# Performance work log

Measured on AMD Instinct MI355X. Metric: run time of the kernel, lower is better.

## Reference

```python
import jax, jax.numpy as jnp
import numpy as np


def setup_inputs() -> dict:
    key = jax.random.key(0)
    ks = jax.random.split(key, 9)
    B = 1024
    s = 0.05
    return {
        "x": jax.random.normal(ks[0], (B, 1024), dtype=jnp.float32),
        "u1": jax.random.normal(ks[1], (8, 8, 16), dtype=jnp.float32) * s,
        "u2": jax.random.normal(ks[2], (8, 8, 16), dtype=jnp.float32) * s,
        "u3": jax.random.normal(ks[3], (16, 16, 16), dtype=jnp.float32) * s,
        "b2": jax.random.normal(ks[4], (16, 16, 16), dtype=jnp.float32) * s,
        "b1_core": jax.random.normal(ks[5], (16, 16), dtype=jnp.float32) * s,
        "bias1": jax.random.normal(ks[6], (8, 8, 16), dtype=jnp.float32) * s,
        "fc2_w": jax.random.normal(ks[7], (10, 1024), dtype=jnp.float32) * s,
        "fc2_b": jax.random.normal(ks[8], (10,), dtype=jnp.float32) * s,
    }


def reference(x, u1, u2, u3, b2, b1_core, bias1, fc2_w, fc2_b):
    batch = x.shape[0]
    t = x.reshape(batch, 8, 8, 16)                       # z a b c
    t = jnp.einsum('zabc,ade->zbcde', t, u1)             # (z,8,16,8,16)
    t = jnp.einsum('zabcd,def->zabcef', t, b2)           # (z,8,16,8,16,16)
    t = jnp.einsum('zabcde,afd->zbcef', t, u2)           # (z,16,8,16,8)
    t = jnp.einsum('zabcd,ce->zabde', t, b1_core)        # (z,16,8,8,16)
    t = jnp.einsum('zabcd,aed->zbce', t, u3)             # (z,8,8,16)
    t = t + bias1
    h = jax.nn.relu(t.reshape(batch, 1024))
    return h @ fc2_w.T + fc2_b
```

## Files before the change

kernel.cpp:

```cpp
#include <hip/hip_runtime.h>


using s16x8 = __attribute__((ext_vector_type(8))) short;
using f32x4 = __attribute__((ext_vector_type(4))) float;

__device__ inline short f2bf(float f) {
    unsigned u = __builtin_bit_cast(unsigned, f);
    u += 0x7fffu + ((u >> 16) & 1u);
    return (short)(u >> 16);
}

__global__ __launch_bounds__(256) void k_build_w(
    const float* __restrict__ u1, const float* __restrict__ u2,
    const float* __restrict__ u3, const float* __restrict__ b2,
    const float* __restrict__ b1c, const float* __restrict__ fc2b,
    short* __restrict__ Wb, float* __restrict__ out) {
    const int blk = blockIdx.x;
    const int tid = threadIdx.x;
    if (blk >= 256) {
        int idx = (blk - 256) * 256 + tid;
        out[idx] = fc2b[idx % 10];
        return;
    }
    __shared__ float b1s[256];
    __shared__ float C2f[4096];
    __shared__ float T1s[256];
    __shared__ float T2s[1024];
    const int ad = blk >> 2, quarter = blk & 3;
    b1s[tid] = b1c[tid];
    __syncthreads();
    for (int j = 0; j < 16; ++j) {
        int idx = tid + 256 * j;
        int e = idx >> 8, p = (idx >> 4) & 15, s = idx & 15;
        float acc = 0.f;
#pragma unroll
        for (int q = 0; q < 16; ++q)
            acc += b2[e * 256 + p * 16 + q] * b1s[q * 16 + s];
        C2f[idx] = acc;
    }
    __syncthreads();
    {
        float acc = 0.f;
#pragma unroll
        for (int e = 0; e < 16; ++e)
            acc += u1[ad * 16 + e] * C2f[e * 256 + tid];
        T1s[tid] = acc;
    }
    __syncthreads();
    for (int j = 0; j < 4; ++j) {
        int idx = tid + 256 * j;
        int s = idx & 15, r = (idx >> 4) & 7, b = idx >> 7;
        float acc = 0.f;
#pragma unroll
        for (int p = 0; p < 16; ++p)
            acc += T1s[p * 16 + s] * u2[(b * 8 + r) * 16 + p];
        T2s[idx] = acc;
    }
    __syncthreads();
    const int a = ad >> 3, d = ad & 7;
    const int rt = quarter * 32 + (tid >> 3);
    const int r = rt >> 4, t = rt & 15;
    const int b = tid & 7;
    const float* t2p = &T2s[(b * 8 + r) * 16];
    short* wrow = &Wb[(d * 128 + rt) * 1024 + a * 128 + b * 16];
    s16x8 v0, v1;
#pragma unroll
    for (int c = 0; c < 16; ++c) {
        const float* u3p = &u3[c * 256 + t * 16];
        float acc = 0.f;
#pragma unroll
        for (int s = 0; s < 16; ++s) acc += t2p[s] * u3p[s];
        short bf = f2bf(acc);
        if (c < 8) v0[c] = bf; else v1[c - 8] = bf;
    }
    *(s16x8*)(wrow) = v0;
    *(s16x8*)(wrow + 8) = v1;
}

#define LDK 136

__global__ __launch_bounds__(256) void k_gemm(
    const float* __restrict__ X, const short* __restrict__ Wb,
    const float* __restrict__ bias, const float* __restrict__ W2,
    float* __restrict__ out) {
    __shared__ short As[64][LDK];
    __shared__ short Bs[64][LDK];
    __shared__ float W2s[10][64];
    const int tid = threadIdx.x;
    const int lane = tid & 63;
    const int w = tid >> 6, wr = w >> 1, wc = w & 1;
    const int z0 = blockIdx.y * 64, o0 = blockIdx.x * 64;
    const int srow = tid >> 2;
    const int sc = (tid & 3) * 16;

    if (tid < 160) {
        int jj = (tid * 4) >> 6, c = (tid * 4) & 63;
        *(float4*)&W2s[jj][c] = *(const float4*)&W2[jj * 1024 + o0 + c];
    }

    const float* xp = &X[(z0 + srow) * 1024 + sc];
    const short* wp = &Wb[(o0 + srow) * 1024 + sc];

    f32x4 acc[2][2] = {};
    float4 ax[8];
    s16x8 bx[4];

#pragma unroll
    for (int h = 0; h < 2; ++h) {
#pragma unroll
        for (int q = 0; q < 4; ++q) ax[h * 4 + q] = *(const float4*)(xp + h * 64 + q * 4);
#pragma unroll
        for (int q = 0; q < 2; ++q) bx[h * 2 + q] = *(const s16x8*)(wp + h * 64 + q * 8);
    }

    for (int k0 = 0; k0 < 1024; k0 += 128) {
#pragma unroll
        for (int h = 0; h < 2; ++h) {
#pragma unroll
            for (int q = 0; q < 2; ++q) {
                float4 lo = ax[h * 4 + 2 * q], hi = ax[h * 4 + 2 * q + 1];
                s16x8 v;
                v[0] = f2bf(lo.x); v[1] = f2bf(lo.y);
                v[2] = f2bf(lo.z); v[3] = f2bf(lo.w);
                v[4] = f2bf(hi.x); v[5] = f2bf(hi.y);
                v[6] = f2bf(hi.z); v[7] = f2bf(hi.w);
                *(s16x8*)&As[srow][sc + h * 64 + q * 8] = v;
                *(s16x8*)&Bs[srow][sc + h * 64 + q * 8] = bx[h * 2 + q];
            }
        }
        __syncthreads();
        if (k0 + 128 < 1024) {
            const float* xi = xp + k0 + 128;
            const short* wi = wp + k0 + 128;
#pragma unroll
            for (int h = 0; h < 2; ++h) {
#pragma unroll
                for (int q = 0; q < 4; ++q) ax[h * 4 + q] = *(const float4*)(xi + h * 64 + q * 4);
#pragma unroll
                for (int q = 0; q < 2; ++q) bx[h * 2 + q] = *(const s16x8*)(wi + h * 64 + q * 8);
            }
        }
#pragma unroll
        for (int ks = 0; ks < 4; ++ks) {
            const int kb = ks * 32 + (lane >> 4) * 8;
            s16x8 a0 = *(const s16x8*)&As[wr * 32 + (lane & 15)][kb];
            s16x8 a1 = *(const s16x8*)&As[wr * 32 + 16 + (lane & 15)][kb];
            s16x8 b0 = *(const s16x8*)&Bs[wc * 32 + (lane & 15)][kb];
            s16x8 b1 = *(const s16x8*)&Bs[wc * 32 + 16 + (lane & 15)][kb];
            acc[0][0] = __builtin_amdgcn_mfma_f32_16x16x32_bf16(a0, b0, acc[0][0], 0, 0, 0);
            acc[0][1] = __builtin_amdgcn_mfma_f32_16x16x32_bf16(a0, b1, acc[0][1], 0, 0, 0);
            acc[1][0] = __builtin_amdgcn_mfma_f32_16x16x32_bf16(a1, b0, acc[1][0], 0, 0, 0);
            acc[1][1] = __builtin_amdgcn_mfma_f32_16x16x32_bf16(a1, b1, acc[1][1], 0, 0, 0);
        }
        __syncthreads();
    }

    float* Ht = (float*)As;
#pragma unroll
    for (int m = 0; m < 2; ++m) {
#pragma unroll
        for (int n = 0; n < 2; ++n) {
            const int row = wr * 32 + m * 16 + (lane >> 4) * 4;
            const int col = wc * 32 + n * 16 + (lane & 15);
            const float bv = bias[o0 + col];
#pragma unroll
            for (int j = 0; j < 4; ++j)
                Ht[(row + j) * 68 + col] = fmaxf(acc[m][n][j] + bv, 0.f);
        }
    }
    __syncthreads();

    const int rrow = tid >> 2, q = tid & 3;
    float part[10];
#pragma unroll
    for (int jj = 0; jj < 10; ++jj) part[jj] = 0.f;
#pragma unroll
    for (int cc = 0; cc < 16; ++cc) {
        const int c = q + 4 * cc;
        const float hv = Ht[rrow * 68 + c];
#pragma unroll
        for (int jj = 0; jj < 10; ++jj) part[jj] += hv * W2s[jj][c];
    }
#pragma unroll
    for (int jj = 0; jj < 10; ++jj) {
        float p = part[jj];
        p += __shfl_xor(p, 1);
        p += __shfl_xor(p, 2);
        if (q == 0) atomicAdd(&out[(z0 + rrow) * 10 + jj], p);
    }
}

extern "C" void kernel_launch(void* const* d_in, const int* in_sizes, int n_in,
                              void* d_out, int out_size, void* d_ws, size_t ws_size,
                              hipStream_t stream) {
    const float* x     = (const float*)d_in[0];
    const float* u1    = (const float*)d_in[1];
    const float* u2    = (const float*)d_in[2];
    const float* u3    = (const float*)d_in[3];
    const float* b2    = (const float*)d_in[4];
    const float* b1c   = (const float*)d_in[5];
    const float* bias1 = (const float*)d_in[6];
    const float* fc2w  = (const float*)d_in[7];
    const float* fc2b  = (const float*)d_in[8];
    float* out = (float*)d_out;

    short* Wb = (short*)d_ws;

    k_build_w<<<296, 256, 0, stream>>>(u1, u2, u3, b2, b1c, fc2b, Wb, out);
    k_gemm<<<dim3(16, 16), 256, 0, stream>>>(x, Wb, bias1, fc2w, out);
}
```

Measured before the change: 32.21 us.

## Fuse weight build and GEMM into one cooperative kernel with grid sync

Merges the weight-construction kernel and the bf16 MFMA GEMM into a single cooperative launch of 256 blocks, separated by a grid-wide barrier. It also repartitions the weight build so each block produces four full rows of the combined matrix, reusing shared memory from the GEMM tiles. The goal is to remove one kernel launch and the gap between dependent kernels. In exchange it pays for a grid sync and redundant per-block recomputation of the small b2·b1 contraction, and it relies on all 256 blocks being co-resident.

Result: slower. 99.91 us (+210.1%).

```diff
diff --git a/kernel.cpp b/kernel.cpp
--- a/kernel.cpp
+++ b/kernel.cpp
@@ -1,4 +1,7 @@
 #include <hip/hip_runtime.h>
+#include <hip/hip_cooperative_groups.h>
+
+namespace cg = cooperative_groups;
 
 
 using s16x8 = __attribute__((ext_vector_type(8))) short;
@@ -10,95 +13,101 @@
     return (short)(u >> 16);
 }
 
-__global__ __launch_bounds__(256) void k_build_w(
-    const float* __restrict__ u1, const float* __restrict__ u2,
-    const float* __restrict__ u3, const float* __restrict__ b2,
-    const float* __restrict__ b1c, const float* __restrict__ fc2b,
-    short* __restrict__ Wb, float* __restrict__ out) {
-    const int blk = blockIdx.x;
-    const int tid = threadIdx.x;
-    if (blk >= 256) {
-        int idx = (blk - 256) * 256 + tid;
-        out[idx] = fc2b[idx % 10];
-        return;
-    }
-    __shared__ float b1s[256];
-    __shared__ float C2f[4096];
-    __shared__ float T1s[256];
-    __shared__ float T2s[1024];
-    const int ad = blk >> 2, quarter = blk & 3;
-    b1s[tid] = b1c[tid];
-    __syncthreads();
-    for (int j = 0; j < 16; ++j) {
-        int idx = tid + 256 * j;
-        int e = idx >> 8, p = (idx >> 4) & 15, s = idx & 15;
-        float acc = 0.f;
-#pragma unroll
-        for (int q = 0; q < 16; ++q)
-            acc += b2[e * 256 + p * 16 + q] * b1s[q * 16 + s];
-        C2f[idx] = acc;
-    }
-    __syncthreads();
-    {
-        float acc = 0.f;
-#pragma unroll
-        for (int e = 0; e < 16; ++e)
-            acc += u1[ad * 16 + e] * C2f[e * 256 + tid];
-        T1s[tid] = acc;
-    }
-    __syncthreads();
-    for (int j = 0; j < 4; ++j) {
-        int idx = tid + 256 * j;
-        int s = idx & 15, r = (idx >> 4) & 7, b = idx >> 7;
-        float acc = 0.f;
-#pragma unroll
-        for (int p = 0; p < 16; ++p)
-            acc += T1s[p * 16 + s] * u2[(b * 8 + r) * 16 + p];
-        T2s[idx] = acc;
-    }
-    __syncthreads();
-    const int a = ad >> 3, d = ad & 7;
-    const int rt = quarter * 32 + (tid >> 3);
-    const int r = rt >> 4, t = rt & 15;
-    const int b = tid & 7;
-    const float* t2p = &T2s[(b * 8 + r) * 16];
-    short* wrow = &Wb[(d * 128 + rt) * 1024 + a * 128 + b * 16];
-    s16x8 v0, v1;
-#pragma unroll
-    for (int c = 0; c < 16; ++c) {
-        const float* u3p = &u3[c * 256 + t * 16];
-        float acc = 0.f;
-#pragma unroll
-        for (int s = 0; s < 16; ++s) acc += t2p[s] * u3p[s];
-        short bf = f2bf(acc);
-        if (c < 8) v0[c] = bf; else v1[c - 8] = bf;
-    }
-    *(s16x8*)(wrow) = v0;
-    *(s16x8*)(wrow + 8) = v1;
-}
-
 #define LDK 136
 
-__global__ __launch_bounds__(256) void k_gemm(
-    const float* __restrict__ X, const short* __restrict__ Wb,
-    const float* __restrict__ bias, const float* __restrict__ W2,
+__global__ __launch_bounds__(256) void k_fused(
+    const float* __restrict__ x, const float* __restrict__ u1,
+    const float* __restrict__ u2, const float* __restrict__ u3,
+    const float* __restrict__ b2, const float* __restrict__ b1c,
+    const float* __restrict__ bias1, const float* __restrict__ fc2w,
+    const float* __restrict__ fc2b, short* __restrict__ Wb,
     float* __restrict__ out) {
     __shared__ short As[64][LDK];
     __shared__ short Bs[64][LDK];
     __shared__ float W2s[10][64];
     const int tid = threadIdx.x;
+    const int blk = blockIdx.x;
+
+    {
+        float* C2f = (float*)As;
+        float* T1s = (float*)Bs;
+        float* T2s = ((float*)Bs) + 2048;
+        const int d = blk >> 5;
+        const int r = (blk >> 2) & 7;
+        const int t0 = (blk & 3) * 4;
+
+        if (tid < 40) {
+            int idx = blk * 40 + tid;
+            out[idx] = fc2b[idx % 10];
+        }
+#pragma unroll
+        for (int j = 0; j < 16; ++j) {
+            int idx = tid + 256 * j;
+            int p = (idx >> 4) & 15, s = idx & 15;
+            float acc = 0.f;
+#pragma unroll
+            for (int q = 0; q < 16; ++q)
+                acc += b2[j * 256 + p * 16 + q] * b1c[q * 16 + s];
+            C2f[idx] = acc;
+        }
+        __syncthreads();
+#pragma unroll
+        for (int j = 0; j < 8; ++j) {
+            float acc = 0.f;
+#pragma unroll
+            for (int e = 0; e < 16; ++e)
+                acc += u1[(j * 8 + d) * 16 + e] * C2f[e * 256 + tid];
+            T1s[j * 256 + tid] = acc;
+        }
+        __syncthreads();
+#pragma unroll
+        for (int j = 0; j < 4; ++j) {
+            int idx = tid + 256 * j;
+            int ab = idx >> 4, s = idx & 15;
+            int a = ab >> 3, b = ab & 7;
+            float acc = 0.f;
+#pragma unroll
+            for (int p = 0; p < 16; ++p)
+                acc += T1s[a * 256 + p * 16 + s] * u2[(b * 8 + r) * 16 + p];
+            T2s[ab * 17 + s] = acc;
+        }
+        __syncthreads();
+        {
+            const int j = tid >> 6;
+            const int t = t0 + j;
+            const int col0 = (tid & 63) * 16;
+            const int ab = col0 >> 4;
+            const float* t2p = &T2s[ab * 17];
+            short* wrow = &Wb[(blk * 4 + j) * 1024 + col0];
+            s16x8 v0, v1;
+#pragma unroll
+            for (int c = 0; c < 16; ++c) {
+                const float* u3p = &u3[c * 256 + t * 16];
+                float acc = 0.f;
+#pragma unroll
+                for (int s = 0; s < 16; ++s) acc += t2p[s] * u3p[s];
+                short bf = f2bf(acc);
+                if (c < 8) v0[c] = bf; else v1[c - 8] = bf;
+            }
+            *(s16x8*)(wrow) = v0;
+            *(s16x8*)(wrow + 8) = v1;
+        }
+    }
+    __threadfence();
+    cg::this_grid().sync();
+
     const int lane = tid & 63;
     const int w = tid >> 6, wr = w >> 1, wc = w & 1;
-    const int z0 = blockIdx.y * 64, o0 = blockIdx.x * 64;
+    const int z0 = (blk >> 4) * 64, o0 = (blk & 15) * 64;
     const int srow = tid >> 2;
     const int sc = (tid & 3) * 16;
 
     if (tid < 160) {
         int jj = (tid * 4) >> 6, c = (tid * 4) & 63;
-        *(float4*)&W2s[jj][c] = *(const float4*)&W2[jj * 1024 + o0 + c];
-    }
-
-    const float* xp = &X[(z0 + srow) * 1024 + sc];
+        *(float4*)&W2s[jj][c] = *(const float4*)&fc2w[jj * 1024 + o0 + c];
+    }
+
+    const float* xp = &x[(z0 + srow) * 1024 + sc];
     const short* wp = &Wb[(o0 + srow) * 1024 + sc];
 
     f32x4 acc[2][2] = {};
@@ -162,7 +171,7 @@
         for (int n = 0; n < 2; ++n) {
             const int row = wr * 32 + m * 16 + (lane >> 4) * 4;
             const int col = wc * 32 + n * 16 + (lane & 15);
-            const float bv = bias[o0 + col];
+            const float bv = bias1[o0 + col];
 #pragma unroll
             for (int j = 0; j < 4; ++j)
                 Ht[(row + j) * 68 + col] = fmaxf(acc[m][n][j] + bv, 0.f);
@@ -203,9 +212,11 @@
     const float* fc2w  = (const float*)d_in[7];
     const float* fc2b  = (const float*)d_in[8];
     float* out = (float*)d_out;
-
     short* Wb = (short*)d_ws;
 
-    k_build_w<<<296, 256, 0, stream>>>(u1, u2, u3, b2, b1c, fc2b, Wb, out);
-    k_gemm<<<dim3(16, 16), 256, 0, stream>>>(x, Wb, bias1, fc2w, out);
+    void* args[] = {(void*)&x, (void*)&u1, (void*)&u2, (void*)&u3,
+                    (void*)&b2, (void*)&b1c, (void*)&bias1, (void*)&fc2w,
+                    (void*)&fc2b, (void*)&Wb, (void*)&out};
+    hipLaunchCooperativeKernel((void*)k_fused, dim3(256), dim3(256), args, 0,
+                               stream);
 }
```
